# Kernel optimization log

Hardware: AMD Instinct MI355X
Metric: run time of the kernel (lower is better)

## Reference

```python
import jax, jax.numpy as jnp
import numpy as np

B, CIN, COUT, MODES, RES = 64, 64, 64, 16, 8192


def setup_inputs() -> dict:
    key = jax.random.key(0)
    kx, kr, ki = jax.random.split(key, 3)
    scale = 1.0 / (CIN * COUT)
    x = jax.random.normal(kx, (B, CIN, RES), dtype=jnp.float32)
    w_real = jax.random.normal(kr, (CIN, COUT, MODES), dtype=jnp.float32) * scale
    w_imag = jax.random.normal(ki, (CIN, COUT, MODES), dtype=jnp.float32) * scale
    return {"x": x, "w_real": w_real, "w_imag": w_imag}


def reference(x, w_real, w_imag):
    # x: [B, Cin, N] real; weight: [Cin, Cout, modes] complex
    batch, _, n = x.shape
    modes = w_real.shape[-1]
    cout = w_real.shape[1]
    w = w_real + 1j * w_imag
    x_ft = jnp.fft.rfft(x)                      # [B, Cin, N//2+1] complex64
    # single batched complex contraction over all kept modes
    out_modes = jnp.einsum('bim,iom->bom', x_ft[:, :, :modes], w)  # [B, Cout, modes]
    out_ft = jnp.zeros((batch, cout, x_ft.shape[-1]), dtype=out_modes.dtype)
    out_ft = out_ft.at[:, :, :modes].set(out_modes)
    return jnp.fft.irfft(out_ft, n=n)           # [B, Cout, N] real
```

## Files before the change

### kernel.cpp

```cpp
#include <hip/hip_runtime.h>
#include <math.h>


#define B_     64
#define CIN_   64
#define COUT_  64
#define MODES_ 16
#define RES_   8192
#define NA     512
#define PITCH  522

__device__ static constexpr float COS16[16] = {
     1.0f,  0.92387953251128674f,  0.70710678118654752f,  0.38268343236508977f,
     0.0f, -0.38268343236508977f, -0.70710678118654752f, -0.92387953251128674f,
    -1.0f, -0.92387953251128674f, -0.70710678118654752f, -0.38268343236508977f,
     0.0f,  0.38268343236508977f,  0.70710678118654752f,  0.92387953251128674f
};
__device__ static constexpr float SIN16[16] = {
     0.0f,  0.38268343236508977f,  0.70710678118654752f,  0.92387953251128674f,
     1.0f,  0.92387953251128674f,  0.70710678118654752f,  0.38268343236508977f,
     0.0f, -0.38268343236508977f, -0.70710678118654752f, -0.92387953251128674f,
    -1.0f, -0.92387953251128674f, -0.70710678118654752f, -0.38268343236508977f
};

#define W8192 7.66990393942820428e-4f

__global__ __launch_bounds__(256) void kA(const float* __restrict__ x,
                                          float* __restrict__ X) {
    __shared__ float Ts[18 * PITCH];
    __shared__ float P[16][17][2];
    const int row = blockIdx.x;
    const int tid = threadIdx.x;
    const float* __restrict__ xr = x + (size_t)row * RES_;

    float2 m[16];
#pragma unroll
    for (int b = 0; b < 16; ++b)
        m[b] = *(const float2*)(xr + 2 * tid + NA * b);

    float2 x0 = m[0], x8 = m[8];
    float2 ev[8], ov[8];
#pragma unroll
    for (int b = 1; b <= 7; ++b) {
        ev[b].x = m[b].x + m[16 - b].x;  ev[b].y = m[b].y + m[16 - b].y;
        ov[b].x = m[b].x - m[16 - b].x;  ov[b].y = m[b].y - m[16 - b].y;
    }
#pragma unroll
    for (int k = 0; k <= 8; ++k) {
        float sr0 = (k & 1) ? (x0.x - x8.x) : (x0.x + x8.x);
        float sr1 = (k & 1) ? (x0.y - x8.y) : (x0.y + x8.y);
        float si0 = 0.f, si1 = 0.f;
#pragma unroll
        for (int b = 1; b <= 7; ++b) {
            const float cc = COS16[(k * b) & 15];
            const float ss = SIN16[(k * b) & 15];
            sr0 = fmaf(ev[b].x, cc, sr0);
            sr1 = fmaf(ev[b].y, cc, sr1);
            si0 = fmaf(ov[b].x, -ss, si0);
            si1 = fmaf(ov[b].y, -ss, si1);
        }
        *(float2*)&Ts[(2 * k) * PITCH + 2 * tid]     = make_float2(sr0, sr1);
        *(float2*)&Ts[(2 * k + 1) * PITCH + 2 * tid] = make_float2(si0, si1);
    }
    __syncthreads();

    const int k  = tid & 15;
    const int c  = tid >> 4;
    const int kp = (k <= 8) ? k : 16 - k;
    const float sgn = (k <= 8) ? 1.f : -1.f;
    float sA, cA, sB, cB;
    __sincosf((float)(k * c)  * W8192, &sA, &cA);
    __sincosf((float)(k * 16) * W8192, &sB, &cB);
    float wre = cA, wim = -sA;
    const float sre = cB, sim = -sB;
    float accr = 0.f, acci = 0.f;
    const float* __restrict__ Tr = &Ts[(2 * kp) * PITCH + c];
    const float* __restrict__ Ti = &Ts[(2 * kp + 1) * PITCH + c];
#pragma unroll 8
    for (int j = 0; j < 32; ++j) {
        const float tr = Tr[16 * j];
        const float ti = sgn * Ti[16 * j];
        accr = fmaf(wre, tr, fmaf(-wim, ti, accr));
        acci = fmaf(wre, ti, fmaf( wim, tr, acci));
        const float nre = fmaf(wre, sre, -wim * sim);
        wim = fmaf(wre, sim, wim * sre);
        wre = nre;
    }
    P[k][c][0] = accr;
    P[k][c][1] = acci;
    __syncthreads();
    if (tid < 16) {
        float xre = 0.f, xim = 0.f;
#pragma unroll
        for (int c2 = 0; c2 < 16; ++c2) { xre += P[tid][c2][0]; xim += P[tid][c2][1]; }
        *(float2*)&X[row * 32 + 2 * tid] = make_float2(xre, xim);
    }
}

__global__ __launch_bounds__(256) void kC(const float* __restrict__ X,
                                          const float* __restrict__ wr,
                                          const float* __restrict__ wi,
                                          float* __restrict__ y) {
    __shared__ float Xs[CIN_ * 32];
    __shared__ float Ps[16][17][2];
    __shared__ float Csh[32];
    const int row = blockIdx.x;
    const int b = row >> 6, o = row & 63;
    const int tid = threadIdx.x;

    const float4* __restrict__ Xb4 = (const float4*)(X + (size_t)b * CIN_ * 32);
    for (int t = tid; t < CIN_ * 8; t += 256)
        ((float4*)Xs)[t] = Xb4[t];
    __syncthreads();

    {
        const int k = tid & 15, p = tid >> 4;
        float pr = 0.f, pi = 0.f;
#pragma unroll
        for (int mI = 0; mI < 4; ++mI) {
            const int i = 4 * p + mI;
            const float xre = Xs[i * 32 + 2 * k];
            const float xim = Xs[i * 32 + 2 * k + 1];
            const float wrv = wr[(i * COUT_ + o) * MODES_ + k];
            const float wiv = wi[(i * COUT_ + o) * MODES_ + k];
            pr = fmaf(xre, wrv, fmaf(-xim, wiv, pr));
            pi = fmaf(xre, wiv, fmaf( xim, wrv, pi));
        }
        Ps[k][p][0] = pr;
        Ps[k][p][1] = pi;
    }
    __syncthreads();
    if (tid < 32) {
        const int k = tid & 15, comp = tid >> 4;
        float s = 0.f;
#pragma unroll
        for (int p = 0; p < 16; ++p) s += Ps[k][p][comp];
        const float g = (k == 0) ? (1.0f / RES_) : (2.0f / RES_);
        Csh[2 * k + comp] = g * s;
    }
    __syncthreads();

    float C[32];
#pragma unroll
    for (int q = 0; q < 8; ++q) {
        const float4 v = ((const float4*)Csh)[q];
        C[4 * q] = v.x; C[4 * q + 1] = v.y; C[4 * q + 2] = v.z; C[4 * q + 3] = v.w;
    }

    float* __restrict__ yr = y + (size_t)row * RES_;
    float yv[16][2];
#pragma unroll
    for (int half = 0; half < 2; ++half) {
        const int a = 2 * tid + half;
        float su, cu;
        __sincosf((float)a * W8192, &su, &cu);
        float wre = 1.f, wim = 0.f;
        float Er0 = 0.f, Er8 = 0.f, Er[8], Oi[8];
#pragma unroll
        for (int q = 1; q <= 7; ++q) { Er[q] = 0.f; Oi[q] = 0.f; }
#pragma unroll
        for (int k = 0; k < 16; ++k) {
            const float cre = C[2 * k], cim = C[2 * k + 1];
            const float dre = fmaf(cre, wre, -cim * wim);
            const float dim = fmaf(cre, wim,  cim * wre);
            if (k == 0)      { Er0 = dre; }
            else if (k == 8) { Er8 = dre; }
            else if (k < 8)  { Er[k]      += dre; Oi[k]      += dim; }
            else             { Er[16 - k] += dre; Oi[16 - k] -= dim; }
            const float nre = fmaf(wre, cu, -wim * su);
            wim = fmaf(wre, su, wim * cu);
            wre = nre;
        }
#pragma unroll
        for (int bb = 0; bb <= 8; ++bb) {
            float Cc = (bb & 1) ? (Er0 - Er8) : (Er0 + Er8);
            float Ss = 0.f;
#pragma unroll
            for (int q = 1; q <= 7; ++q) {
                Cc = fmaf(Er[q], COS16[(q * bb) & 15], Cc);
                Ss = fmaf(Oi[q], SIN16[(q * bb) & 15], Ss);
            }
            if (bb == 0)      yv[0][half] = Cc;
            else if (bb == 8) yv[8][half] = Cc;
            else { yv[bb][half] = Cc - Ss; yv[16 - bb][half] = Cc + Ss; }
        }
    }
#pragma unroll
    for (int bb = 0; bb < 16; ++bb)
        *(float2*)(yr + NA * bb + 2 * tid) = make_float2(yv[bb][0], yv[bb][1]);
}

extern "C" void kernel_launch(void* const* d_in, const int* in_sizes, int n_in,
                              void* d_out, int out_size, void* d_ws, size_t ws_size,
                              hipStream_t stream) {
    const float* x  = (const float*)d_in[0];
    const float* wr = (const float*)d_in[1];
    const float* wi = (const float*)d_in[2];
    float* out = (float*)d_out;
    float* X = (float*)d_ws;

    kA<<<dim3(B_ * CIN_), dim3(256), 0, stream>>>(x, X);
    kC<<<dim3(B_ * COUT_), dim3(256), 0, stream>>>(X, wr, wi, out);
}
```

Baseline: 240.5 us.

## Fuse forward DFT and spectral inverse into one cooperative persistent kernel

Replaces the two launches with a single cooperative kernel that runs a persistent grid over rows. It computes the truncated forward DFT, synchronises the grid, then does the mode mixing and inverse transform. Twiddle setup is hoisted out of the row loops, and the X tile is reloaded only when the batch index changes. This removes one launch and the inter-kernel gap, at the cost of grid.sync overhead and lower per-row parallelism. The shared-memory pitch also changes, which alters the LDS bank pattern.

```diff
diff --git a/kernel.cpp b/kernel.cpp
--- a/kernel.cpp
+++ b/kernel.cpp
@@ -1,4 +1,5 @@
 #include <hip/hip_runtime.h>
+#include <hip/hip_cooperative_groups.h>
 #include <math.h>
 
 
@@ -8,7 +9,10 @@
 #define MODES_ 16
 #define RES_   8192
 #define NA     512
-#define PITCH  522
+#define PITCH  514
+#define NROW   4096
+
+namespace cg = cooperative_groups;
 
 __device__ static constexpr float COS16[16] = {
      1.0f,  0.92387953251128674f,  0.70710678118654752f,  0.38268343236508977f,
@@ -25,19 +29,202 @@
 
 #define W8192 7.66990393942820428e-4f
 
+struct SharedA {
+    float Ts[18 * PITCH];
+    float P[16][17][2];
+};
+struct SharedC {
+    float Xs[CIN_ * 32];
+    float Ps[16][17][2];
+    float Csh[32];
+};
+union SharedU { SharedA a; SharedC c; };
+
+__global__ __launch_bounds__(256, 4) void fused(const float* __restrict__ x,
+                                                const float* __restrict__ wr,
+                                                const float* __restrict__ wi,
+                                                float* __restrict__ X,
+                                                float* __restrict__ y) {
+    cg::grid_group grid = cg::this_grid();
+    __shared__ SharedU sh;
+    const int tid = threadIdx.x;
+    const int R  = (NROW + gridDim.x - 1) / gridDim.x;
+    const int r0 = blockIdx.x * R;
+    const int r1 = (r0 + R < NROW) ? (r0 + R) : NROW;
+
+    const int k  = tid & 15;
+    const int c  = tid >> 4;
+    const int kp = (k <= 8) ? k : 16 - k;
+    const float sgn = (k <= 8) ? 1.f : -1.f;
+    float sA, cA, sB, cB;
+    __sincosf((float)(k * c)  * W8192, &sA, &cA);
+    __sincosf((float)(k * 16) * W8192, &sB, &cB);
+    const float wre0 = cA, wim0 = -sA;
+    const float sre = cB, sim = -sB;
+
+    for (int row = r0; row < r1; ++row) {
+        const float* __restrict__ xr = x + (size_t)row * RES_;
+        float2 m[16];
+#pragma unroll
+        for (int b = 0; b < 16; ++b)
+            m[b] = *(const float2*)(xr + 2 * tid + NA * b);
+        float2 x0 = m[0], x8 = m[8];
+        float2 ev[8], ov[8];
+#pragma unroll
+        for (int b = 1; b <= 7; ++b) {
+            ev[b].x = m[b].x + m[16 - b].x;  ev[b].y = m[b].y + m[16 - b].y;
+            ov[b].x = m[b].x - m[16 - b].x;  ov[b].y = m[b].y - m[16 - b].y;
+        }
+#pragma unroll
+        for (int kk = 0; kk <= 8; ++kk) {
+            float sr0 = (kk & 1) ? (x0.x - x8.x) : (x0.x + x8.x);
+            float sr1 = (kk & 1) ? (x0.y - x8.y) : (x0.y + x8.y);
+            float si0 = 0.f, si1 = 0.f;
+#pragma unroll
+            for (int b = 1; b <= 7; ++b) {
+                const float cc = COS16[(kk * b) & 15];
+                const float ss = SIN16[(kk * b) & 15];
+                sr0 = fmaf(ev[b].x, cc, sr0);
+                sr1 = fmaf(ev[b].y, cc, sr1);
+                si0 = fmaf(ov[b].x, -ss, si0);
+                si1 = fmaf(ov[b].y, -ss, si1);
+            }
+            *(float2*)&sh.a.Ts[(2 * kk) * PITCH + 2 * tid]     = make_float2(sr0, sr1);
+            *(float2*)&sh.a.Ts[(2 * kk + 1) * PITCH + 2 * tid] = make_float2(si0, si1);
+        }
+        __syncthreads();
+
+        float wre = wre0, wim = wim0;
+        float accr = 0.f, acci = 0.f;
+        const float* __restrict__ Tr = &sh.a.Ts[(2 * kp) * PITCH + c];
+        const float* __restrict__ Ti = &sh.a.Ts[(2 * kp + 1) * PITCH + c];
+#pragma unroll 8
+        for (int j = 0; j < 32; ++j) {
+            const float tr = Tr[16 * j];
+            const float ti = sgn * Ti[16 * j];
+            accr = fmaf(wre, tr, fmaf(-wim, ti, accr));
+            acci = fmaf(wre, ti, fmaf( wim, tr, acci));
+            const float nre = fmaf(wre, sre, -wim * sim);
+            wim = fmaf(wre, sim, wim * sre);
+            wre = nre;
+        }
+        sh.a.P[k][c][0] = accr;
+        sh.a.P[k][c][1] = acci;
+        __syncthreads();
+        if (tid < 16) {
+            float xre = 0.f, xim = 0.f;
+#pragma unroll
+            for (int c2 = 0; c2 < 16; ++c2) { xre += sh.a.P[tid][c2][0]; xim += sh.a.P[tid][c2][1]; }
+            *(float2*)&X[row * 32 + 2 * tid] = make_float2(xre, xim);
+        }
+        __syncthreads();
+    }
+
+    grid.sync();
+
+    float su0, cu0, su1, cu1;
+    __sincosf((float)(2 * tid)     * W8192, &su0, &cu0);
+    __sincosf((float)(2 * tid + 1) * W8192, &su1, &cu1);
+
+    int curb = -1;
+    for (int row = r0; row < r1; ++row) {
+        const int b = row >> 6, o = row & 63;
+        if (b != curb) {
+            __syncthreads();
+            const float4* __restrict__ Xb4 = (const float4*)(X + (size_t)b * CIN_ * 32);
+            for (int t = tid; t < CIN_ * 8; t += 256)
+                ((float4*)sh.c.Xs)[t] = Xb4[t];
+            __syncthreads();
+            curb = b;
+        }
+
+        {
+            const int kk = tid & 15, p = tid >> 4;
+            float pr = 0.f, pi = 0.f;
+#pragma unroll
+            for (int mI = 0; mI < 4; ++mI) {
+                const int i = 4 * p + mI;
+                const float xre = sh.c.Xs[i * 32 + 2 * kk];
+                const float xim = sh.c.Xs[i * 32 + 2 * kk + 1];
+                const float wrv = wr[(i * COUT_ + o) * MODES_ + kk];
+                const float wiv = wi[(i * COUT_ + o) * MODES_ + kk];
+                pr = fmaf(xre, wrv, fmaf(-xim, wiv, pr));
+                pi = fmaf(xre, wiv, fmaf( xim, wrv, pi));
+            }
+            sh.c.Ps[kk][p][0] = pr;
+            sh.c.Ps[kk][p][1] = pi;
+        }
+        __syncthreads();
+        if (tid < 32) {
+            const int kk = tid & 15, comp = tid >> 4;
+            float s = 0.f;
+#pragma unroll
+            for (int p = 0; p < 16; ++p) s += sh.c.Ps[kk][p][comp];
+            const float g = (kk == 0) ? (1.0f / RES_) : (2.0f / RES_);
+            sh.c.Csh[2 * kk + comp] = g * s;
+        }
+        __syncthreads();
+
+        float C[32];
+#pragma unroll
+        for (int q = 0; q < 8; ++q) {
+            const float4 v = ((const float4*)sh.c.Csh)[q];
+            C[4 * q] = v.x; C[4 * q + 1] = v.y; C[4 * q + 2] = v.z; C[4 * q + 3] = v.w;
+        }
+
+        float* __restrict__ yr = y + (size_t)row * RES_;
+        float yv[16][2];
+#pragma unroll
+        for (int half = 0; half < 2; ++half) {
+            const float su = half ? su1 : su0;
+            const float cu = half ? cu1 : cu0;
+            float wre = 1.f, wim = 0.f;
+            float Er0 = 0.f, Er8 = 0.f, Er[8], Oi[8];
+#pragma unroll
+            for (int q = 1; q <= 7; ++q) { Er[q] = 0.f; Oi[q] = 0.f; }
+#pragma unroll
+            for (int kk = 0; kk < 16; ++kk) {
+                const float cre = C[2 * kk], cim = C[2 * kk + 1];
+                const float dre = fmaf(cre, wre, -cim * wim);
+                const float dim = fmaf(cre, wim,  cim * wre);
+                if (kk == 0)      { Er0 = dre; }
+                else if (kk == 8) { Er8 = dre; }
+                else if (kk < 8)  { Er[kk]      += dre; Oi[kk]      += dim; }
+                else              { Er[16 - kk] += dre; Oi[16 - kk] -= dim; }
+                const float nre = fmaf(wre, cu, -wim * su);
+                wim = fmaf(wre, su, wim * cu);
+                wre = nre;
+            }
+#pragma unroll
+            for (int bb = 0; bb <= 8; ++bb) {
+                float Cc = (bb & 1) ? (Er0 - Er8) : (Er0 + Er8);
+                float Ss = 0.f;
+#pragma unroll
+                for (int q = 1; q <= 7; ++q) {
+                    Cc = fmaf(Er[q], COS16[(q * bb) & 15], Cc);
+                    Ss = fmaf(Oi[q], SIN16[(q * bb) & 15], Ss);
+                }
+                if (bb == 0)      yv[0][half] = Cc;
+                else if (bb == 8) yv[8][half] = Cc;
+                else { yv[bb][half] = Cc - Ss; yv[16 - bb][half] = Cc + Ss; }
+            }
+        }
+#pragma unroll
+        for (int bb = 0; bb < 16; ++bb)
+            *(float2*)(yr + NA * bb + 2 * tid) = make_float2(yv[bb][0], yv[bb][1]);
+        __syncthreads();
+    }
+}
+
 __global__ __launch_bounds__(256) void kA(const float* __restrict__ x,
                                           float* __restrict__ X) {
-    __shared__ float Ts[18 * PITCH];
-    __shared__ float P[16][17][2];
+    __shared__ SharedA sa;
     const int row = blockIdx.x;
     const int tid = threadIdx.x;
     const float* __restrict__ xr = x + (size_t)row * RES_;
-
     float2 m[16];
 #pragma unroll
-    for (int b = 0; b < 16; ++b)
-        m[b] = *(const float2*)(xr + 2 * tid + NA * b);
-
+    for (int b = 0; b < 16; ++b) m[b] = *(const float2*)(xr + 2 * tid + NA * b);
     float2 x0 = m[0], x8 = m[8];
     float2 ev[8], ov[8];
 #pragma unroll
@@ -46,26 +233,24 @@
         ov[b].x = m[b].x - m[16 - b].x;  ov[b].y = m[b].y - m[16 - b].y;
     }
 #pragma unroll
-    for (int k = 0; k <= 8; ++k) {
-        float sr0 = (k & 1) ? (x0.x - x8.x) : (x0.x + x8.x);
-        float sr1 = (k & 1) ? (x0.y - x8.y) : (x0.y + x8.y);
+    for (int kk = 0; kk <= 8; ++kk) {
+        float sr0 = (kk & 1) ? (x0.x - x8.x) : (x0.x + x8.x);
+        float sr1 = (kk & 1) ? (x0.y - x8.y) : (x0.y + x8.y);
         float si0 = 0.f, si1 = 0.f;
 #pragma unroll
         for (int b = 1; b <= 7; ++b) {
-            const float cc = COS16[(k * b) & 15];
-            const float ss = SIN16[(k * b) & 15];
+            const float cc = COS16[(kk * b) & 15];
+            const float ss = SIN16[(kk * b) & 15];
             sr0 = fmaf(ev[b].x, cc, sr0);
             sr1 = fmaf(ev[b].y, cc, sr1);
             si0 = fmaf(ov[b].x, -ss, si0);
             si1 = fmaf(ov[b].y, -ss, si1);
         }
-        *(float2*)&Ts[(2 * k) * PITCH + 2 * tid]     = make_float2(sr0, sr1);
-        *(float2*)&Ts[(2 * k + 1) * PITCH + 2 * tid] = make_float2(si0, si1);
-    }
-    __syncthreads();
-
-    const int k  = tid & 15;
-    const int c  = tid >> 4;
+        *(float2*)&sa.Ts[(2 * kk) * PITCH + 2 * tid]     = make_float2(sr0, sr1);
+        *(float2*)&sa.Ts[(2 * kk + 1) * PITCH + 2 * tid] = make_float2(si0, si1);
+    }
+    __syncthreads();
+    const int k = tid & 15, c = tid >> 4;
     const int kp = (k <= 8) ? k : 16 - k;
     const float sgn = (k <= 8) ? 1.f : -1.f;
     float sA, cA, sB, cB;
@@ -74,8 +259,8 @@
     float wre = cA, wim = -sA;
     const float sre = cB, sim = -sB;
     float accr = 0.f, acci = 0.f;
-    const float* __restrict__ Tr = &Ts[(2 * kp) * PITCH + c];
-    const float* __restrict__ Ti = &Ts[(2 * kp + 1) * PITCH + c];
+    const float* __restrict__ Tr = &sa.Ts[(2 * kp) * PITCH + c];
+    const float* __restrict__ Ti = &sa.Ts[(2 * kp + 1) * PITCH + c];
 #pragma unroll 8
     for (int j = 0; j < 32; ++j) {
         const float tr = Tr[16 * j];
@@ -86,13 +271,13 @@
         wim = fmaf(wre, sim, wim * sre);
         wre = nre;
     }
-    P[k][c][0] = accr;
-    P[k][c][1] = acci;
+    sa.P[k][c][0] = accr;
+    sa.P[k][c][1] = acci;
     __syncthreads();
     if (tid < 16) {
         float xre = 0.f, xim = 0.f;
 #pragma unroll
-        for (int c2 = 0; c2 < 16; ++c2) { xre += P[tid][c2][0]; xim += P[tid][c2][1]; }
+        for (int c2 = 0; c2 < 16; ++c2) { xre += sa.P[tid][c2][0]; xim += sa.P[tid][c2][1]; }
         *(float2*)&X[row * 32 + 2 * tid] = make_float2(xre, xim);
     }
 }
@@ -101,52 +286,45 @@
                                           const float* __restrict__ wr,
                                           const float* __restrict__ wi,
                                           float* __restrict__ y) {
-    __shared__ float Xs[CIN_ * 32];
-    __shared__ float Ps[16][17][2];
-    __shared__ float Csh[32];
+    __shared__ SharedC sc;
     const int row = blockIdx.x;
     const int b = row >> 6, o = row & 63;
     const int tid = threadIdx.x;
-
     const float4* __restrict__ Xb4 = (const float4*)(X + (size_t)b * CIN_ * 32);
-    for (int t = tid; t < CIN_ * 8; t += 256)
-        ((float4*)Xs)[t] = Xb4[t];
-    __syncthreads();
-
+    for (int t = tid; t < CIN_ * 8; t += 256) ((float4*)sc.Xs)[t] = Xb4[t];
+    __syncthreads();
     {
-        const int k = tid & 15, p = tid >> 4;
+        const int kk = tid & 15, p = tid >> 4;
         float pr = 0.f, pi = 0.f;
 #pragma unroll
         for (int mI = 0; mI < 4; ++mI) {
             const int i = 4 * p + mI;
-            const float xre = Xs[i * 32 + 2 * k];
-            const float xim = Xs[i * 32 + 2 * k + 1];
-            const float wrv = wr[(i * COUT_ + o) * MODES_ + k];
-            const float wiv = wi[(i * COUT_ + o) * MODES_ + k];
+            const float xre = sc.Xs[i * 32 + 2 * kk];
+            const float xim = sc.Xs[i * 32 + 2 * kk + 1];
+            const float wrv = wr[(i * COUT_ + o) * MODES_ + kk];
+            const float wiv = wi[(i * COUT_ + o) * MODES_ + kk];
             pr = fmaf(xre, wrv, fmaf(-xim, wiv, pr));
             pi = fmaf(xre, wiv, fmaf( xim, wrv, pi));
         }
-        Ps[k][p][0] = pr;
-        Ps[k][p][1] = pi;
+        sc.Ps[kk][p][0] = pr;
+        sc.Ps[kk][p][1] = pi;
     }
     __syncthreads();
     if (tid < 32) {
-        const int k = tid & 15, comp = tid >> 4;
+        const int kk = tid & 15, comp = tid >> 4;
         float s = 0.f;
 #pragma unroll
-        for (int p = 0; p < 16; ++p) s += Ps[k][p][comp];
-        const float g = (k == 0) ? (1.0f / RES_) : (2.0f / RES_);
-        Csh[2 * k + comp] = g * s;
-    }
-    __syncthreads();
-
+        for (int p = 0; p < 16; ++p) s += sc.Ps[kk][p][comp];
+        const float g = (kk == 0) ? (1.0f / RES_) : (2.0f / RES_);
+        sc.Csh[2 * kk + comp] = g * s;
+    }
+    __syncthreads();
     float C[32];
 #pragma unroll
     for (int q = 0; q < 8; ++q) {
-        const float4 v = ((const float4*)Csh)[q];
+        const float4 v = ((const float4*)sc.Csh)[q];
         C[4 * q] = v.x; C[4 * q + 1] = v.y; C[4 * q + 2] = v.z; C[4 * q + 3] = v.w;
     }
-
     float* __restrict__ yr = y + (size_t)row * RES_;
     float yv[16][2];
 #pragma unroll
@@ -159,14 +337,14 @@
 #pragma unroll
         for (int q = 1; q <= 7; ++q) { Er[q] = 0.f; Oi[q] = 0.f; }
 #pragma unroll
-        for (int k = 0; k < 16; ++k) {
-            const float cre = C[2 * k], cim = C[2 * k + 1];
+        for (int kk = 0; kk < 16; ++kk) {
+            const float cre = C[2 * kk], cim = C[2 * kk + 1];
             const float dre = fmaf(cre, wre, -cim * wim);
             const float dim = fmaf(cre, wim,  cim * wre);
-            if (k == 0)      { Er0 = dre; }
-            else if (k == 8) { Er8 = dre; }
-            else if (k < 8)  { Er[k]      += dre; Oi[k]      += dim; }
-            else             { Er[16 - k] += dre; Oi[16 - k] -= dim; }
+            if (kk == 0)      { Er0 = dre; }
+            else if (kk == 8) { Er8 = dre; }
+            else if (kk < 8)  { Er[kk]      += dre; Oi[kk]      += dim; }
+            else              { Er[16 - kk] += dre; Oi[16 - kk] -= dim; }
             const float nre = fmaf(wre, cu, -wim * su);
             wim = fmaf(wre, su, wim * cu);
             wre = nre;
@@ -199,6 +377,17 @@
     float* out = (float*)d_out;
     float* X = (float*)d_ws;
 
-    kA<<<dim3(B_ * CIN_), dim3(256), 0, stream>>>(x, X);
-    kC<<<dim3(B_ * COUT_), dim3(256), 0, stream>>>(X, wr, wi, out);
+    int nb = 0;
+    (void)hipOccupancyMaxActiveBlocksPerMultiprocessor(&nb, fused, 256, 0);
+    if (nb < 1) nb = 1;
+    int gridn = nb * 256;
+    if (gridn > 1024) gridn = 1024;
+
+    void* args[] = {(void*)&x, (void*)&wr, (void*)&wi, (void*)&X, (void*)&out};
+    hipError_t err = hipLaunchCooperativeKernel((const void*)fused, dim3(gridn),
+                                                dim3(256), args, 0, stream);
+    if (err != hipSuccess) {
+        kA<<<dim3(B_ * CIN_), dim3(256), 0, stream>>>(x, X);
+        kC<<<dim3(B_ * COUT_), dim3(256), 0, stream>>>(X, wr, wi, out);
+    }
 }
```

New measurement: 318.9 us. 1.33x slower.
